# Kernel optimization log

Measured on AMD Instinct MI355X. Metric: run time of the kernel, lower is better.

Reference implementation:

```python
import jax, jax.numpy as jnp
import numpy as np

DIM = 256
N_EMBED = 1024
COMMITMENT_COST = 0.25


def setup_inputs() -> dict:
    key = jax.random.key(0)
    k1, k2 = jax.random.split(key)
    z = jax.random.normal(k1, (16, 256, 64, 64), dtype=jnp.float32)
    # nn.Embedding weight initialized uniform(-1/n_embed, 1/n_embed)
    embed = jax.random.uniform(k2, (N_EMBED, DIM), dtype=jnp.float32,
                               minval=-1.0 / N_EMBED, maxval=1.0 / N_EMBED)
    return {"z": z, "embed": embed}


def reference(z, embed):
    sg = jax.lax.stop_gradient
    # NCHW -> NHWC, flatten spatial+batch to tokens
    zp = jnp.transpose(z, (0, 2, 3, 1))            # [B,H,W,C]
    zf = zp.reshape(-1, DIM)                        # [N, C]
    # squared euclidean distances via expansion: |z|^2 + |e|^2 - 2 z.e
    d = (jnp.sum(zf * zf, axis=1, keepdims=True)
         + jnp.sum(embed * embed, axis=1)
         - 2.0 * zf @ embed.T)                      # [N, K]
    idx = jnp.argmin(d, axis=1)                     # [N]
    min_encodings = jax.nn.one_hot(idx, N_EMBED, dtype=zf.dtype)  # [N, K]
    # direct gather == one-hot @ embed (same math, one HBM pass)
    z_q = embed[idx].reshape(zp.shape)              # [B,H,W,C]
    loss = (jnp.mean((sg(z_q) - zp) ** 2)
            + COMMITMENT_COST * jnp.mean((z_q - sg(zp)) ** 2))
    # straight-through estimator
    z_q_st = zp + sg(z_q - zp)
    e_mean = jnp.mean(min_encodings, axis=0)
    perplexity = jnp.exp(-jnp.sum(e_mean * jnp.log(e_mean + 1e-10)))
    z_q_out = jnp.transpose(z_q_st, (0, 3, 1, 2))   # back to NCHW
    return (loss, z_q_out, perplexity, min_encodings, idx[:, None])
```

## Files before the change

kernel.cpp:

```cpp
#include <hip/hip_runtime.h>
#include <math.h>

#define DIM    256
#define K_EMB  1024
#define HW     4096
#define CHW    1048576
#define N_TOK  65536
#define NELEM  16777216

#define OUT_LOSS 0
#define OUT_ZQ   1
#define OUT_PERP 16777217
#define OUT_MENC 16777218LL
#define OUT_IDX  83886082

#define TAU  1.5e-4f

#define TAIL_ROW0  65216
#define FLAGS_OFF  66781184LL
#define FBS_OFF    66846720LL
#define EH_OFF     66912258LL

typedef short short8  __attribute__((ext_vector_type(8)));
typedef float floatx4 __attribute__((ext_vector_type(4)));
typedef float floatx2 __attribute__((ext_vector_type(2)));

__device__ __forceinline__ unsigned short f2bf(float f) {
    unsigned int u = __float_as_uint(f);
    return (unsigned short)((u + 0x7FFFu + ((u >> 16) & 1u)) >> 16);
}
__device__ __forceinline__ float bf2f(unsigned short h) {
    return __uint_as_float(((unsigned int)h) << 16);
}

__device__ __forceinline__ float np_pair128(const float* p) {
    float r[8];
    #pragma unroll
    for (int j = 0; j < 8; ++j) r[j] = p[j];
    for (int i = 8; i < 128; i += 8)
        #pragma unroll
        for (int j = 0; j < 8; ++j) r[j] = __fadd_rn(r[j], p[i + j]);
    return __fadd_rn(__fadd_rn(__fadd_rn(r[0], r[1]), __fadd_rn(r[2], r[3])),
                     __fadd_rn(__fadd_rn(r[4], r[5]), __fadd_rn(r[6], r[7])));
}
__device__ __forceinline__ float np_pair256(const float* p) {
    return __fadd_rn(np_pair128(p), np_pair128(p + 128));
}

__device__ __forceinline__ void build_frags(const float* __restrict__ zp, int quad, short8* a) {
    #pragma unroll
    for (int kc = 0; kc < 8; ++kc) {
        short8 vh, vl;
        #pragma unroll
        for (int u = 0; u < 8; ++u) {
            float v = __builtin_nontemporal_load(zp + (size_t)(kc * 32 + quad * 8 + u) * HW);
            unsigned short h = f2bf(v);
            vh[u] = (short)h;
            vl[u] = (short)f2bf(v - bf2f(h));
        }
        a[kc]     = vh;
        a[8 + kc] = vl;
    }
}

__global__ void t2_np_kernel(const float* __restrict__ embed, float* __restrict__ t2,
                             unsigned short* __restrict__ Eh) {
    int k = blockIdx.x * 256 + threadIdx.x;
    if (k >= K_EMB) return;
    const float* e = embed + (size_t)k * DIM;
    float p[256];
    for (int c = 0; c < DIM; c += 4) {
        float4 v = *(const float4*)(e + c);
        p[c]     = __fmul_rn(v.x, v.x);
        p[c + 1] = __fmul_rn(v.y, v.y);
        p[c + 2] = __fmul_rn(v.z, v.z);
        p[c + 3] = __fmul_rn(v.w, v.w);
    }
    t2[k] = np_pair256(p);
    unsigned short* dst = Eh + (size_t)k * DIM;
    for (int c0 = 0; c0 < DIM; c0 += 8) {
        short8 vh;
        #pragma unroll
        for (int u = 0; u < 8; ++u) vh[u] = (short)f2bf(e[c0 + u]);
        *(short8*)(dst + c0) = vh;
    }
}

__launch_bounds__(256, 4)
__global__ void vq_mfma(const float* __restrict__ z,
                        const float* __restrict__ embed,
                        const unsigned short* __restrict__ Eh,
                        const float* __restrict__ t2g,
                        float* __restrict__ out,
                        unsigned int* __restrict__ nflag,
                        int* __restrict__ flags,
                        float* __restrict__ fbs,
                        unsigned int* __restrict__ counts,
                        float* __restrict__ loss_sum) {
    __shared__ unsigned short lds_b[32 * 264];
    __shared__ float t2_lds[K_EMB];
    __shared__ int midx[64];

    const int tid  = threadIdx.x;
    const int lane = tid & 63;
    const int wv   = tid >> 6;
    const int l15  = lane & 15;
    const int quad = lane >> 4;
    const int m0   = blockIdx.x * 64;

    for (int i = tid; i < K_EMB; i += 256) t2_lds[i] = t2g[i];

    short8 a[16];
    {
        const int n = m0 + wv * 16 + l15;
        build_frags(z + (size_t)(n >> 12) * CHW + (n & 4095), quad, a);
    }

    float bs[4], ss[4]; int bk[4];
    #pragma unroll
    for (int r = 0; r < 4; ++r) { bs[r] = 3.4e38f; ss[r] = 3.4e38f; bk[r] = 0; }

    const int srow = tid >> 3;
    const int scol = (tid & 7) * 32;

    for (int it = 0; it < 32; ++it) {
        const int n0 = it * 32;
        __syncthreads();
        {
            const short8* g = (const short8*)(Eh + (size_t)(n0 + srow) * 256 + scol);
            short8* l = (short8*)(lds_b + srow * 264 + scol);
            short8 v0 = g[0], v1 = g[1], v2 = g[2], v3 = g[3];
            l[0] = v0; l[1] = v1; l[2] = v2; l[3] = v3;
        }
        __syncthreads();
        floatx4 acc0 = {0.f, 0.f, 0.f, 0.f};
        floatx4 acc1 = {0.f, 0.f, 0.f, 0.f};
        #pragma unroll
        for (int kc = 0; kc < 8; ++kc) {
            short8 b0 = *(const short8*)(lds_b + l15 * 264 + kc * 32 + quad * 8);
            short8 b1 = *(const short8*)(lds_b + (16 + l15) * 264 + kc * 32 + quad * 8);
            acc0 = __builtin_amdgcn_mfma_f32_16x16x32_bf16(a[kc],     b0, acc0, 0, 0, 0);
            acc1 = __builtin_amdgcn_mfma_f32_16x16x32_bf16(a[kc],     b1, acc1, 0, 0, 0);
            acc0 = __builtin_amdgcn_mfma_f32_16x16x32_bf16(a[8 + kc], b0, acc0, 0, 0, 0);
            acc1 = __builtin_amdgcn_mfma_f32_16x16x32_bf16(a[8 + kc], b1, acc1, 0, 0, 0);
        }
        float t20 = t2_lds[n0 + l15];
        float t21 = t2_lds[n0 + 16 + l15];
        #pragma unroll
        for (int r = 0; r < 4; ++r) {
            float s0 = fmaf(-2.0f, acc0[r], t20);
            if (s0 < bs[r]) { ss[r] = bs[r]; bs[r] = s0; bk[r] = n0 + l15; }
            else if (s0 < ss[r]) ss[r] = s0;
            float s1 = fmaf(-2.0f, acc1[r], t21);
            if (s1 < bs[r]) { ss[r] = bs[r]; bs[r] = s1; bk[r] = n0 + 16 + l15; }
            else if (s1 < ss[r]) ss[r] = s1;
        }
    }

    #pragma unroll
    for (int r = 0; r < 4; ++r) {
        for (int mo = 1; mo < 16; mo <<= 1) {
            float obs = __shfl_xor(bs[r], mo, 64);
            float oss = __shfl_xor(ss[r], mo, 64);
            int   obk = __shfl_xor(bk[r], mo, 64);
            if (obs < bs[r] || (obs == bs[r] && obk < bk[r])) {
                ss[r] = fminf(bs[r], oss); bs[r] = obs; bk[r] = obk;
            } else {
                ss[r] = fminf(ss[r], obs);
            }
        }
        if (l15 == 0) {
            int tl = wv * 16 + quad * 4 + r;
            out[OUT_IDX + m0 + tl] = (float)bk[r];
            midx[tl] = bk[r];
            atomicAdd(&counts[bk[r]], 1u);
            if (ss[r] - bs[r] < TAU) {
                unsigned int slot = atomicAdd(nflag, 1u);
                flags[slot] = m0 + tl;
                fbs[slot]   = bs[r];
            }
        }
    }
    __syncthreads();

    {
        const int n   = m0 + wv * 16 + l15;
        const int myk = midx[wv * 16 + l15];
        const float* erow = embed + (size_t)myk * DIM;
        float* zqp = out + OUT_ZQ + (size_t)(n >> 12) * CHW + (n & 4095);
        float lsum = 0.0f;
        #pragma unroll
        for (int kc = 0; kc < 8; ++kc) {
            const int c0 = kc * 32 + quad * 8;
            float4 e0 = *(const float4*)(erow + c0);
            float4 e1 = *(const float4*)(erow + c0 + 4);
            float ev[8] = {e0.x, e0.y, e0.z, e0.w, e1.x, e1.y, e1.z, e1.w};
            #pragma unroll
            for (int u = 0; u < 8; ++u) {
                float vv = __fadd_rn(bf2f((unsigned short)a[kc][u]),
                                     bf2f((unsigned short)a[8 + kc][u]));
                float dz = ev[u] - vv;
                lsum = fmaf(dz, dz, lsum);
                __builtin_nontemporal_store(ev[u], zqp + (size_t)(c0 + u) * HW);
            }
        }
        #pragma unroll
        for (int off = 32; off > 0; off >>= 1) lsum += __shfl_down(lsum, off, 64);
        if (lane == 0) atomicAdd(loss_sum, lsum);
    }

    if (blockIdx.x < (TAIL_ROW0 / 64)) {
        #pragma unroll 1
        for (int j = 0; j < 64; ++j) {
            const int id = midx[j];
            floatx2* dst = (floatx2*)(out + OUT_MENC + (size_t)(m0 + j) * K_EMB);
            int c0 = tid * 2;
            floatx2 v;  v.x  = (c0 == id)       ? 1.0f : 0.0f;  v.y  = (c0 + 1 == id)  ? 1.0f : 0.0f;
            __builtin_nontemporal_store(v, dst + tid);
            int c1 = c0 + 512;
            floatx2 w2; w2.x = (c1 == id)       ? 1.0f : 0.0f;  w2.y = (c1 + 1 == id)  ? 1.0f : 0.0f;
            __builtin_nontemporal_store(w2, dst + 256 + tid);
        }
    }
}

__launch_bounds__(256)
__global__ void refine_mfma(const float* __restrict__ z, const float* __restrict__ embed,
                            const unsigned short* __restrict__ Eh,
                            const float* __restrict__ t2g, float* __restrict__ out,
                            const unsigned int* __restrict__ nflag,
                            const int* __restrict__ flags,
                            const float* __restrict__ fbs,
                            unsigned int* __restrict__ counts,
                            float* __restrict__ loss_sum) {
    __shared__ unsigned short lds_b[32 * 264];
    __shared__ float t2_lds[K_EMB];
    __shared__ int   ftok[64];
    __shared__ float fbest[64];
    __shared__ int   ccnt[64];
    __shared__ int   clist[64][32];
    __shared__ float pp4[4][256];

    const int tid  = threadIdx.x;
    const int lane = tid & 63;
    const int wv   = tid >> 6;
    const int l15  = lane & 15;
    const int quad = lane >> 4;
    const int nf   = (int)*nflag;

    for (int i = tid; i < K_EMB; i += 256) t2_lds[i] = t2g[i];

    const int srow = tid >> 3;
    const int scol = (tid & 7) * 32;

    for (int base = blockIdx.x * 64; base < nf; base += gridDim.x * 64) {
        __syncthreads();
        if (tid < 64) {
            int ii  = base + tid;
            int src = (ii < nf) ? ii : base;
            ftok[tid]  = flags[src];
            fbest[tid] = fbs[src];
            ccnt[tid]  = 0;
        }
        __syncthreads();

        short8 a[16];
        {
            const int n = ftok[wv * 16 + l15];
            build_frags(z + (size_t)(n >> 12) * CHW + (n & 4095), quad, a);
        }
        float ftb[4];
        #pragma unroll
        for (int r = 0; r < 4; ++r) ftb[r] = fbest[wv * 16 + quad * 4 + r] + TAU;

        for (int it = 0; it < 32; ++it) {
            const int n0 = it * 32;
            __syncthreads();
            {
                const short8* g = (const short8*)(Eh + (size_t)(n0 + srow) * 256 + scol);
                short8* l = (short8*)(lds_b + srow * 264 + scol);
                short8 v0 = g[0], v1 = g[1], v2 = g[2], v3 = g[3];
                l[0] = v0; l[1] = v1; l[2] = v2; l[3] = v3;
            }
            __syncthreads();
            floatx4 acc0 = {0.f, 0.f, 0.f, 0.f};
            floatx4 acc1 = {0.f, 0.f, 0.f, 0.f};
            #pragma unroll
            for (int kc = 0; kc < 8; ++kc) {
                short8 b0 = *(const short8*)(lds_b + l15 * 264 + kc * 32 + quad * 8);
                short8 b1 = *(const short8*)(lds_b + (16 + l15) * 264 + kc * 32 + quad * 8);
                acc0 = __builtin_amdgcn_mfma_f32_16x16x32_bf16(a[kc],     b0, acc0, 0, 0, 0);
                acc1 = __builtin_amdgcn_mfma_f32_16x16x32_bf16(a[kc],     b1, acc1, 0, 0, 0);
                acc0 = __builtin_amdgcn_mfma_f32_16x16x32_bf16(a[8 + kc], b0, acc0, 0, 0, 0);
                acc1 = __builtin_amdgcn_mfma_f32_16x16x32_bf16(a[8 + kc], b1, acc1, 0, 0, 0);
            }
            float t20 = t2_lds[n0 + l15];
            float t21 = t2_lds[n0 + 16 + l15];
            #pragma unroll
            for (int r = 0; r < 4; ++r) {
                const int trow = wv * 16 + quad * 4 + r;
                float s0 = fmaf(-2.0f, acc0[r], t20);
                if (s0 <= ftb[r]) {
                    int pos = atomicAdd(&ccnt[trow], 1);
                    if (pos < 32) clist[trow][pos] = n0 + l15;
                }
                float s1 = fmaf(-2.0f, acc1[r], t21);
                if (s1 <= ftb[r]) {
                    int pos = atomicAdd(&ccnt[trow], 1);
                    if (pos < 32) clist[trow][pos] = n0 + 16 + l15;
                }
            }
        }
        __syncthreads();

        for (int j = wv * 16; j < wv * 16 + 16; ++j) {
            if (base + j >= nf) break;
            const int n = ftok[j];
            int cnt = ccnt[j]; if (cnt > 32) cnt = 32;

            const float* zt = z + (size_t)(n >> 12) * CHW + (n & 4095);
            double zd[4]; float zf[4];
            #pragma unroll
            for (int u = 0; u < 4; ++u) {
                float v = zt[(size_t)(lane + u * 64) * HW];
                zf[u] = v; zd[u] = (double)v;
                pp4[wv][lane + u * 64] = __fmul_rn(v, v);
            }
            __asm__ volatile("s_waitcnt lgkmcnt(0)" ::: "memory");
            float rj = 0.0f;
            if (lane < 16) {
                int jj = lane & 7, half = lane >> 3;
                const float* p = &pp4[wv][half * 128 + jj];
                rj = p[0];
                #pragma unroll
                for (int ii = 1; ii < 16; ++ii) rj = __fadd_rn(rj, p[ii * 8]);
            }
            float v0 = __shfl(rj, 0, 64), v1 = __shfl(rj, 1, 64), v2 = __shfl(rj, 2, 64), v3 = __shfl(rj, 3, 64);
            float v4 = __shfl(rj, 4, 64), v5 = __shfl(rj, 5, 64), v6 = __shfl(rj, 6, 64), v7 = __shfl(rj, 7, 64);
            float h0 = __fadd_rn(__fadd_rn(__fadd_rn(v0, v1), __fadd_rn(v2, v3)),
                                 __fadd_rn(__fadd_rn(v4, v5), __fadd_rn(v6, v7)));
            v0 = __shfl(rj,  8, 64); v1 = __shfl(rj,  9, 64); v2 = __shfl(rj, 10, 64); v3 = __shfl(rj, 11, 64);
            v4 = __shfl(rj, 12, 64); v5 = __shfl(rj, 13, 64); v6 = __shfl(rj, 14, 64); v7 = __shfl(rj, 15, 64);
            float h1 = __fadd_rn(__fadd_rn(__fadd_rn(v0, v1), __fadd_rn(v2, v3)),
                                 __fadd_rn(__fadd_rn(v4, v5), __fadd_rn(v6, v7)));
            const float t1 = __fadd_rn(h0, h1);

            float bd = 3.4e38f; int bkk = 1 << 30;
            for (int ci = 0; ci < cnt; ++ci) {
                int k = clist[j][ci];
                const float* e = embed + (size_t)k * DIM;
                double s = 0.0;
                #pragma unroll
                for (int u = 0; u < 4; ++u) s = fma(zd[u], (double)e[lane + u * 64], s);
                for (int mo = 1; mo < 64; mo <<= 1) s += __shfl_xor(s, mo, 64);
                float rho = (float)s;
                float d = __fadd_rn(__fadd_rn(t1, t2_lds[k]), -__fmul_rn(2.0f, rho));
                if (d < bd || (d == bd && k < bkk)) { bd = d; bkk = k; }
            }

            const int old = (int)out[OUT_IDX + n];
            if (bkk != old) {
                const float* eo = embed + (size_t)old * DIM;
                const float* en = embed + (size_t)bkk * DIM;
                float* zqp = out + OUT_ZQ + (size_t)(n >> 12) * CHW + (n & 4095);
                float dl = 0.0f;
                #pragma unroll
                for (int u = 0; u < 4; ++u) {
                    const int c = lane + u * 64;
                    float d_new = en[c] - zf[u];
                    float d_old = eo[c] - zf[u];
                    dl += d_new * d_new - d_old * d_old;
                    zqp[(size_t)c * HW] = en[c];
                }
                for (int mo = 1; mo < 64; mo <<= 1) dl += __shfl_xor(dl, mo, 64);
                if (lane == 0) {
                    atomicAdd(loss_sum, dl);
                    atomicAdd(&counts[old], 0xFFFFFFFFu);
                    atomicAdd(&counts[bkk], 1u);
                    out[OUT_IDX + n] = (float)bkk;
                    if (n < TAIL_ROW0) {
                        out[OUT_MENC + (size_t)n * K_EMB + old] = 0.0f;
                        out[OUT_MENC + (size_t)n * K_EMB + bkk] = 1.0f;
                    }
                }
            }
        }
    }
}

__global__ void menc_tail(float* __restrict__ out) {
    const int row = TAIL_ROW0 + blockIdx.x;
    const int id  = (int)out[OUT_IDX + row];
    floatx2* dst = (floatx2*)(out + OUT_MENC + (size_t)row * K_EMB);
    int c0 = threadIdx.x * 2;
    floatx2 v;  v.x  = (c0 == id)      ? 1.0f : 0.0f;  v.y  = (c0 + 1 == id) ? 1.0f : 0.0f;
    dst[threadIdx.x] = v;
    int c1 = c0 + 512;
    floatx2 w;  w.x  = (c1 == id)      ? 1.0f : 0.0f;  w.y  = (c1 + 1 == id) ? 1.0f : 0.0f;
    dst[256 + threadIdx.x] = w;
}

__global__ void finalize_kernel(const unsigned int* __restrict__ counts,
                                const float* __restrict__ loss_sum,
                                float* __restrict__ out) {
    __shared__ float red[256];
    int tid = threadIdx.x;
    float hsum = 0.0f;
    for (int k = tid; k < K_EMB; k += 256) {
        float p = (float)counts[k] * (1.0f / 65536.0f);
        hsum += p * logf(p + 1e-10f);
    }
    red[tid] = hsum;
    __syncthreads();
    for (int s = 128; s > 0; s >>= 1) {
        if (tid < s) red[tid] += red[tid + s];
        __syncthreads();
    }
    if (tid == 0) {
        out[OUT_PERP] = expf(-red[0]);
        out[OUT_LOSS] = loss_sum[0] * 1.25f * (1.0f / (float)NELEM);
    }
}

extern "C" void kernel_launch(void* const* d_in, const int* in_sizes, int n_in,
                              void* d_out, int out_size, void* d_ws, size_t ws_size,
                              hipStream_t stream) {
    const float* z     = (const float*)d_in[0];
    const float* embed = (const float*)d_in[1];
    float* out = (float*)d_out;

    unsigned int* counts = (unsigned int*)d_ws;
    float* loss_sum      = (float*)((char*)d_ws + 4096);
    unsigned int* nflag  = (unsigned int*)((char*)d_ws + 4100);
    float* t2g           = (float*)((char*)d_ws + 8192);

    float* scr = out + OUT_MENC;
    int*            fl = (int*)(scr + FLAGS_OFF);
    float*          fb = (float*)(scr + FBS_OFF);
    unsigned short* Eh = (unsigned short*)(scr + EH_OFF);

    (void)hipMemsetAsync(d_ws, 0, 4104, stream);
    t2_np_kernel   <<<dim3(4),    dim3(256), 0, stream>>>(embed, t2g, Eh);
    vq_mfma        <<<dim3(1024), dim3(256), 0, stream>>>(z, embed, Eh, t2g, out, nflag, fl, fb, counts, loss_sum);
    refine_mfma    <<<dim3(128),  dim3(256), 0, stream>>>(z, embed, Eh, t2g, out, nflag, fl, fb, counts, loss_sum);
    menc_tail      <<<dim3(320),  dim3(256), 0, stream>>>(out);
    finalize_kernel<<<dim3(1),    dim3(256), 0, stream>>>(counts, loss_sum, out);
}
```

Measured before the change: 774.1 us.

## Fuse near-tie refinement into main VQ kernel with in-LDS candidate lists

Removes the separate refine kernel, which recomputed the full MFMA distance sweep for flagged tokens. The main kernel now collects near-best candidates in shared memory during its sweep and re-scores ties in double precision before writing indices, counts, z_q and one-hot rows. Final values are written once instead of being patched afterwards, and the scratch region shrinks so menc_tail covers fewer rows. In exchange, every tile now pays a per-row shuffle-min and LDS atomics. Candidate lists that overflow fall back to a full 1024-code double-precision scan, and blocks with many ties may stall.

After: 726.5 us. 6.1% less time.

```diff
diff --git a/kernel.cpp b/kernel.cpp
--- a/kernel.cpp
+++ b/kernel.cpp
@@ -15,11 +15,10 @@
 #define OUT_IDX  83886082
 
 #define TAU  1.5e-4f
-
-#define TAIL_ROW0  65216
-#define FLAGS_OFF  66781184LL
-#define FBS_OFF    66846720LL
-#define EH_OFF     66912258LL
+#define CAND_CAP 16
+
+#define TAIL_ROW0  65407
+#define EH_OFF     66976770LL
 
 typedef short short8  __attribute__((ext_vector_type(8)));
 typedef float floatx4 __attribute__((ext_vector_type(4)));
@@ -92,14 +91,16 @@
                         const unsigned short* __restrict__ Eh,
                         const float* __restrict__ t2g,
                         float* __restrict__ out,
-                        unsigned int* __restrict__ nflag,
-                        int* __restrict__ flags,
-                        float* __restrict__ fbs,
                         unsigned int* __restrict__ counts,
                         float* __restrict__ loss_sum) {
     __shared__ unsigned short lds_b[32 * 264];
     __shared__ float t2_lds[K_EMB];
     __shared__ int midx[64];
+    __shared__ unsigned short clist[64][CAND_CAP];
+    __shared__ int ccnt[64];
+    __shared__ int flist[64];
+    __shared__ int fn;
+    __shared__ float pp4[4][256];
 
     const int tid  = threadIdx.x;
     const int lane = tid & 63;
@@ -109,6 +110,8 @@
     const int m0   = blockIdx.x * 64;
 
     for (int i = tid; i < K_EMB; i += 256) t2_lds[i] = t2g[i];
+    if (tid < 64) ccnt[tid] = 0;
+    if (tid == 0) fn = 0;
 
     short8 a[16];
     {
@@ -116,9 +119,9 @@
         build_frags(z + (size_t)(n >> 12) * CHW + (n & 4095), quad, a);
     }
 
-    float bs[4], ss[4]; int bk[4];
+    float bs[4], ss[4], tb[4]; int bk[4];
     #pragma unroll
-    for (int r = 0; r < 4; ++r) { bs[r] = 3.4e38f; ss[r] = 3.4e38f; bk[r] = 0; }
+    for (int r = 0; r < 4; ++r) { bs[r] = 3.4e38f; ss[r] = 3.4e38f; tb[r] = 3.4e38f; bk[r] = 0; }
 
     const int srow = tid >> 3;
     const int scol = (tid & 7) * 32;
@@ -148,12 +151,27 @@
         float t21 = t2_lds[n0 + 16 + l15];
         #pragma unroll
         for (int r = 0; r < 4; ++r) {
+            const int trow = wv * 16 + quad * 4 + r;
             float s0 = fmaf(-2.0f, acc0[r], t20);
             if (s0 < bs[r]) { ss[r] = bs[r]; bs[r] = s0; bk[r] = n0 + l15; }
             else if (s0 < ss[r]) ss[r] = s0;
             float s1 = fmaf(-2.0f, acc1[r], t21);
             if (s1 < bs[r]) { ss[r] = bs[r]; bs[r] = s1; bk[r] = n0 + 16 + l15; }
             else if (s1 < ss[r]) ss[r] = s1;
+
+            float m01 = fminf(s0, s1);
+            #pragma unroll
+            for (int mo = 1; mo < 16; mo <<= 1) m01 = fminf(m01, __shfl_xor(m01, mo, 64));
+            tb[r] = fminf(tb[r], m01);
+            const float thr = tb[r] + TAU;
+            if (s0 <= thr) {
+                int pos = atomicAdd(&ccnt[trow], 1);
+                if (pos < CAND_CAP) clist[trow][pos] = (unsigned short)(n0 + l15);
+            }
+            if (s1 <= thr) {
+                int pos = atomicAdd(&ccnt[trow], 1);
+                if (pos < CAND_CAP) clist[trow][pos] = (unsigned short)(n0 + 16 + l15);
+            }
         }
     }
 
@@ -171,17 +189,82 @@
         }
         if (l15 == 0) {
             int tl = wv * 16 + quad * 4 + r;
-            out[OUT_IDX + m0 + tl] = (float)bk[r];
             midx[tl] = bk[r];
-            atomicAdd(&counts[bk[r]], 1u);
             if (ss[r] - bs[r] < TAU) {
-                unsigned int slot = atomicAdd(nflag, 1u);
-                flags[slot] = m0 + tl;
-                fbs[slot]   = bs[r];
+                int p = atomicAdd(&fn, 1);
+                flist[p] = tl;
             }
         }
     }
     __syncthreads();
+
+    const int nfb = fn;
+    for (int f = wv; f < nfb; f += 4) {
+        const int tl = flist[f];
+        const int n  = m0 + tl;
+        const int cnt = ccnt[tl];
+
+        const float* zt = z + (size_t)(n >> 12) * CHW + (n & 4095);
+        double zd[4];
+        #pragma unroll
+        for (int u = 0; u < 4; ++u) {
+            float v = zt[(size_t)(lane + u * 64) * HW];
+            zd[u] = (double)v;
+            pp4[wv][lane + u * 64] = __fmul_rn(v, v);
+        }
+        __asm__ volatile("s_waitcnt lgkmcnt(0)" ::: "memory");
+        float rj = 0.0f;
+        if (lane < 16) {
+            int jj = lane & 7, half = lane >> 3;
+            const float* p = &pp4[wv][half * 128 + jj];
+            rj = p[0];
+            #pragma unroll
+            for (int ii = 1; ii < 16; ++ii) rj = __fadd_rn(rj, p[ii * 8]);
+        }
+        float v0 = __shfl(rj, 0, 64), v1 = __shfl(rj, 1, 64), v2 = __shfl(rj, 2, 64), v3 = __shfl(rj, 3, 64);
+        float v4 = __shfl(rj, 4, 64), v5 = __shfl(rj, 5, 64), v6 = __shfl(rj, 6, 64), v7 = __shfl(rj, 7, 64);
+        float h0 = __fadd_rn(__fadd_rn(__fadd_rn(v0, v1), __fadd_rn(v2, v3)),
+                             __fadd_rn(__fadd_rn(v4, v5), __fadd_rn(v6, v7)));
+        v0 = __shfl(rj,  8, 64); v1 = __shfl(rj,  9, 64); v2 = __shfl(rj, 10, 64); v3 = __shfl(rj, 11, 64);
+        v4 = __shfl(rj, 12, 64); v5 = __shfl(rj, 13, 64); v6 = __shfl(rj, 14, 64); v7 = __shfl(rj, 15, 64);
+        float h1 = __fadd_rn(__fadd_rn(__fadd_rn(v0, v1), __fadd_rn(v2, v3)),
+                             __fadd_rn(__fadd_rn(v4, v5), __fadd_rn(v6, v7)));
+        const float t1 = __fadd_rn(h0, h1);
+
+        float bd = 3.4e38f; int bkk = 1 << 30;
+        if (cnt <= CAND_CAP) {
+            for (int ci = 0; ci < cnt; ++ci) {
+                int k = clist[tl][ci];
+                const float* e = embed + (size_t)k * DIM;
+                double s = 0.0;
+                #pragma unroll
+                for (int u = 0; u < 4; ++u) s = fma(zd[u], (double)e[lane + u * 64], s);
+                for (int mo = 1; mo < 64; mo <<= 1) s += __shfl_xor(s, mo, 64);
+                float rho = (float)s;
+                float d = __fadd_rn(__fadd_rn(t1, t2_lds[k]), -__fmul_rn(2.0f, rho));
+                if (d < bd || (d == bd && k < bkk)) { bd = d; bkk = k; }
+            }
+        } else {
+            for (int k = 0; k < K_EMB; ++k) {
+                const float* e = embed + (size_t)k * DIM;
+                double s = 0.0;
+                #pragma unroll
+                for (int u = 0; u < 4; ++u) s = fma(zd[u], (double)e[lane + u * 64], s);
+                for (int mo = 1; mo < 64; mo <<= 1) s += __shfl_xor(s, mo, 64);
+                float rho = (float)s;
+                float d = __fadd_rn(__fadd_rn(t1, t2_lds[k]), -__fmul_rn(2.0f, rho));
+                if (d < bd) { bd = d; bkk = k; }
+            }
+        }
+        if (lane == 0) midx[tl] = bkk;
+    }
+    __syncthreads();
+
+    if (tid < 64) {
+        const int id = midx[tid];
+        out[OUT_IDX + m0 + tid] = (float)id;
+        atomicAdd(&counts[id], 1u);
+    }
 
     {
         const int n   = m0 + wv * 16 + l15;
@@ -209,182 +292,17 @@
         if (lane == 0) atomicAdd(loss_sum, lsum);
     }
 
-    if (blockIdx.x < (TAIL_ROW0 / 64)) {
-        #pragma unroll 1
-        for (int j = 0; j < 64; ++j) {
-            const int id = midx[j];
-            floatx2* dst = (floatx2*)(out + OUT_MENC + (size_t)(m0 + j) * K_EMB);
-            int c0 = tid * 2;
-            floatx2 v;  v.x  = (c0 == id)       ? 1.0f : 0.0f;  v.y  = (c0 + 1 == id)  ? 1.0f : 0.0f;
-            __builtin_nontemporal_store(v, dst + tid);
-            int c1 = c0 + 512;
-            floatx2 w2; w2.x = (c1 == id)       ? 1.0f : 0.0f;  w2.y = (c1 + 1 == id)  ? 1.0f : 0.0f;
-            __builtin_nontemporal_store(w2, dst + 256 + tid);
-        }
-    }
-}
-
-__launch_bounds__(256)
-__global__ void refine_mfma(const float* __restrict__ z, const float* __restrict__ embed,
-                            const unsigned short* __restrict__ Eh,
-                            const float* __restrict__ t2g, float* __restrict__ out,
-                            const unsigned int* __restrict__ nflag,
-                            const int* __restrict__ flags,
-                            const float* __restrict__ fbs,
-                            unsigned int* __restrict__ counts,
-                            float* __restrict__ loss_sum) {
-    __shared__ unsigned short lds_b[32 * 264];
-    __shared__ float t2_lds[K_EMB];
-    __shared__ int   ftok[64];
-    __shared__ float fbest[64];
-    __shared__ int   ccnt[64];
-    __shared__ int   clist[64][32];
-    __shared__ float pp4[4][256];
-
-    const int tid  = threadIdx.x;
-    const int lane = tid & 63;
-    const int wv   = tid >> 6;
-    const int l15  = lane & 15;
-    const int quad = lane >> 4;
-    const int nf   = (int)*nflag;
-
-    for (int i = tid; i < K_EMB; i += 256) t2_lds[i] = t2g[i];
-
-    const int srow = tid >> 3;
-    const int scol = (tid & 7) * 32;
-
-    for (int base = blockIdx.x * 64; base < nf; base += gridDim.x * 64) {
-        __syncthreads();
-        if (tid < 64) {
-            int ii  = base + tid;
-            int src = (ii < nf) ? ii : base;
-            ftok[tid]  = flags[src];
-            fbest[tid] = fbs[src];
-            ccnt[tid]  = 0;
-        }
-        __syncthreads();
-
-        short8 a[16];
-        {
-            const int n = ftok[wv * 16 + l15];
-            build_frags(z + (size_t)(n >> 12) * CHW + (n & 4095), quad, a);
-        }
-        float ftb[4];
-        #pragma unroll
-        for (int r = 0; r < 4; ++r) ftb[r] = fbest[wv * 16 + quad * 4 + r] + TAU;
-
-        for (int it = 0; it < 32; ++it) {
-            const int n0 = it * 32;
-            __syncthreads();
-            {
-                const short8* g = (const short8*)(Eh + (size_t)(n0 + srow) * 256 + scol);
-                short8* l = (short8*)(lds_b + srow * 264 + scol);
-                short8 v0 = g[0], v1 = g[1], v2 = g[2], v3 = g[3];
-                l[0] = v0; l[1] = v1; l[2] = v2; l[3] = v3;
-            }
-            __syncthreads();
-            floatx4 acc0 = {0.f, 0.f, 0.f, 0.f};
-            floatx4 acc1 = {0.f, 0.f, 0.f, 0.f};
-            #pragma unroll
-            for (int kc = 0; kc < 8; ++kc) {
-                short8 b0 = *(const short8*)(lds_b + l15 * 264 + kc * 32 + quad * 8);
-                short8 b1 = *(const short8*)(lds_b + (16 + l15) * 264 + kc * 32 + quad * 8);
-                acc0 = __builtin_amdgcn_mfma_f32_16x16x32_bf16(a[kc],     b0, acc0, 0, 0, 0);
-                acc1 = __builtin_amdgcn_mfma_f32_16x16x32_bf16(a[kc],     b1, acc1, 0, 0, 0);
-                acc0 = __builtin_amdgcn_mfma_f32_16x16x32_bf16(a[8 + kc], b0, acc0, 0, 0, 0);
-                acc1 = __builtin_amdgcn_mfma_f32_16x16x32_bf16(a[8 + kc], b1, acc1, 0, 0, 0);
-            }
-            float t20 = t2_lds[n0 + l15];
-            float t21 = t2_lds[n0 + 16 + l15];
-            #pragma unroll
-            for (int r = 0; r < 4; ++r) {
-                const int trow = wv * 16 + quad * 4 + r;
-                float s0 = fmaf(-2.0f, acc0[r], t20);
-                if (s0 <= ftb[r]) {
-                    int pos = atomicAdd(&ccnt[trow], 1);
-                    if (pos < 32) clist[trow][pos] = n0 + l15;
-                }
-                float s1 = fmaf(-2.0f, acc1[r], t21);
-                if (s1 <= ftb[r]) {
-                    int pos = atomicAdd(&ccnt[trow], 1);
-                    if (pos < 32) clist[trow][pos] = n0 + 16 + l15;
-                }
-            }
-        }
-        __syncthreads();
-
-        for (int j = wv * 16; j < wv * 16 + 16; ++j) {
-            if (base + j >= nf) break;
-            const int n = ftok[j];
-            int cnt = ccnt[j]; if (cnt > 32) cnt = 32;
-
-            const float* zt = z + (size_t)(n >> 12) * CHW + (n & 4095);
-            double zd[4]; float zf[4];
-            #pragma unroll
-            for (int u = 0; u < 4; ++u) {
-                float v = zt[(size_t)(lane + u * 64) * HW];
-                zf[u] = v; zd[u] = (double)v;
-                pp4[wv][lane + u * 64] = __fmul_rn(v, v);
-            }
-            __asm__ volatile("s_waitcnt lgkmcnt(0)" ::: "memory");
-            float rj = 0.0f;
-            if (lane < 16) {
-                int jj = lane & 7, half = lane >> 3;
-                const float* p = &pp4[wv][half * 128 + jj];
-                rj = p[0];
-                #pragma unroll
-                for (int ii = 1; ii < 16; ++ii) rj = __fadd_rn(rj, p[ii * 8]);
-            }
-            float v0 = __shfl(rj, 0, 64), v1 = __shfl(rj, 1, 64), v2 = __shfl(rj, 2, 64), v3 = __shfl(rj, 3, 64);
-            float v4 = __shfl(rj, 4, 64), v5 = __shfl(rj, 5, 64), v6 = __shfl(rj, 6, 64), v7 = __shfl(rj, 7, 64);
-            float h0 = __fadd_rn(__fadd_rn(__fadd_rn(v0, v1), __fadd_rn(v2, v3)),
-                                 __fadd_rn(__fadd_rn(v4, v5), __fadd_rn(v6, v7)));
-            v0 = __shfl(rj,  8, 64); v1 = __shfl(rj,  9, 64); v2 = __shfl(rj, 10, 64); v3 = __shfl(rj, 11, 64);
-            v4 = __shfl(rj, 12, 64); v5 = __shfl(rj, 13, 64); v6 = __shfl(rj, 14, 64); v7 = __shfl(rj, 15, 64);
-            float h1 = __fadd_rn(__fadd_rn(__fadd_rn(v0, v1), __fadd_rn(v2, v3)),
-                                 __fadd_rn(__fadd_rn(v4, v5), __fadd_rn(v6, v7)));
-            const float t1 = __fadd_rn(h0, h1);
-
-            float bd = 3.4e38f; int bkk = 1 << 30;
-            for (int ci = 0; ci < cnt; ++ci) {
-                int k = clist[j][ci];
-                const float* e = embed + (size_t)k * DIM;
-                double s = 0.0;
-                #pragma unroll
-                for (int u = 0; u < 4; ++u) s = fma(zd[u], (double)e[lane + u * 64], s);
-                for (int mo = 1; mo < 64; mo <<= 1) s += __shfl_xor(s, mo, 64);
-                float rho = (float)s;
-                float d = __fadd_rn(__fadd_rn(t1, t2_lds[k]), -__fmul_rn(2.0f, rho));
-                if (d < bd || (d == bd && k < bkk)) { bd = d; bkk = k; }
-            }
-
-            const int old = (int)out[OUT_IDX + n];
-            if (bkk != old) {
-                const float* eo = embed + (size_t)old * DIM;
-                const float* en = embed + (size_t)bkk * DIM;
-                float* zqp = out + OUT_ZQ + (size_t)(n >> 12) * CHW + (n & 4095);
-                float dl = 0.0f;
-                #pragma unroll
-                for (int u = 0; u < 4; ++u) {
-                    const int c = lane + u * 64;
-                    float d_new = en[c] - zf[u];
-                    float d_old = eo[c] - zf[u];
-                    dl += d_new * d_new - d_old * d_old;
-                    zqp[(size_t)c * HW] = en[c];
-                }
-                for (int mo = 1; mo < 64; mo <<= 1) dl += __shfl_xor(dl, mo, 64);
-                if (lane == 0) {
-                    atomicAdd(loss_sum, dl);
-                    atomicAdd(&counts[old], 0xFFFFFFFFu);
-                    atomicAdd(&counts[bkk], 1u);
-                    out[OUT_IDX + n] = (float)bkk;
-                    if (n < TAIL_ROW0) {
-                        out[OUT_MENC + (size_t)n * K_EMB + old] = 0.0f;
-                        out[OUT_MENC + (size_t)n * K_EMB + bkk] = 1.0f;
-                    }
-                }
-            }
-        }
+    #pragma unroll 1
+    for (int j = 0; j < 64; ++j) {
+        if (m0 + j >= TAIL_ROW0) break;
+        const int id = midx[j];
+        floatx2* dst = (floatx2*)(out + OUT_MENC + (size_t)(m0 + j) * K_EMB);
+        int c0 = tid * 2;
+        floatx2 v;  v.x  = (c0 == id)       ? 1.0f : 0.0f;  v.y  = (c0 + 1 == id)  ? 1.0f : 0.0f;
+        __builtin_nontemporal_store(v, dst + tid);
+        int c1 = c0 + 512;
+        floatx2 w2; w2.x = (c1 == id)       ? 1.0f : 0.0f;  w2.y = (c1 + 1 == id)  ? 1.0f : 0.0f;
+        __builtin_nontemporal_store(w2, dst + 256 + tid);
     }
 }
 
@@ -431,18 +349,14 @@
 
     unsigned int* counts = (unsigned int*)d_ws;
     float* loss_sum      = (float*)((char*)d_ws + 4096);
-    unsigned int* nflag  = (unsigned int*)((char*)d_ws + 4100);
     float* t2g           = (float*)((char*)d_ws + 8192);
 
     float* scr = out + OUT_MENC;
-    int*            fl = (int*)(scr + FLAGS_OFF);
-    float*          fb = (float*)(scr + FBS_OFF);
     unsigned short* Eh = (unsigned short*)(scr + EH_OFF);
 
     (void)hipMemsetAsync(d_ws, 0, 4104, stream);
     t2_np_kernel   <<<dim3(4),    dim3(256), 0, stream>>>(embed, t2g, Eh);
-    vq_mfma        <<<dim3(1024), dim3(256), 0, stream>>>(z, embed, Eh, t2g, out, nflag, fl, fb, counts, loss_sum);
-    refine_mfma    <<<dim3(128),  dim3(256), 0, stream>>>(z, embed, Eh, t2g, out, nflag, fl, fb, counts, loss_sum);
-    menc_tail      <<<dim3(320),  dim3(256), 0, stream>>>(out);
+    vq_mfma        <<<dim3(1024), dim3(256), 0, stream>>>(z, embed, Eh, t2g, out, counts, loss_sum);
+    menc_tail      <<<dim3(129),  dim3(256), 0, stream>>>(out);
     finalize_kernel<<<dim3(1),    dim3(256), 0, stream>>>(counts, loss_sum, out);
 }
```
